# Kernel tuning notes

Hardware: AMD Instinct MI355X
Metric: run time of the kernel (lower is better)

## Reference

```python
import jax, jax.numpy as jnp
import numpy as np

MU = 5
ETA = 1.0
ITERATIONS = 3


def _sobel(x):
    # torch F.conv2d is cross-correlation; replicate exactly
    k = jnp.array([[-1., 0., 1.], [-2., 0., 2.], [-1., 0., 1.]], dtype=x.dtype)
    kernel = jnp.stack([k, k.T])[:, None]  # [2,1,3,3] OIHW
    return jax.lax.conv_general_dilated(
        x, kernel, window_strides=(1, 1), padding=[(1, 1), (1, 1)],
        dimension_numbers=('NCHW', 'OIHW', 'NCHW'))


def _cnorm(v):
    # 2-norm over channel dim, keepdim
    return jnp.sqrt(jnp.sum(v * v, axis=1, keepdims=True))


def setup_inputs() -> dict:
    key = jax.random.key(0)
    inputs = jax.random.uniform(key, (8, 1, 1024, 1024), dtype=jnp.float32)
    return {"inputs": inputs}


def reference(inputs):
    B, _, H, W = inputs.shape
    pad = ((0, 0), (0, 0), (MU, MU), (MU, MU))

    sobel = _sobel(inputs)                       # [B,2,H,W]
    sobel_mag = _cnorm(sobel)                    # [B,1,H,W]
    sobel_mag = sobel_mag / jnp.max(sobel_mag)
    sobel_mag_p = jnp.pad(sobel_mag, pad)

    # tang = flip(sobel, ch) * [-1, 1] -> perpendicular (tangent) field
    tang = jnp.stack([-sobel[:, 1], sobel[:, 0]], axis=1)
    tmag = _cnorm(tang)
    tang = tang / jnp.where(tmag == 0, jnp.ones_like(tmag), tmag)

    for _it in range(ITERATIONS):
        for ori in ('V', 'H'):
            tang_p = jnp.pad(tang, pad)
            tang_X = tang
            acc = jnp.zeros_like(tang)
            for i in range(2 * MU + 1):
                if ori == 'V':
                    tang_Y = tang_p[:, :, i:i + H, MU:MU + W]
                    sob_Y = sobel_mag_p[:, :, i:i + H, MU:MU + W]
                else:
                    tang_Y = tang_p[:, :, MU:MU + H, i:i + W]
                    sob_Y = sobel_mag_p[:, :, MU:MU + H, i:i + W]
                w = (jnp.tanh(ETA * (sob_Y - sobel_mag)) + 1.0) \
                    * jnp.sum(tang_X * tang_Y, axis=1, keepdims=True) * 0.5
                acc = acc + tang_Y * w
            tang = acc
        tmag = _cnorm(tang)
        tang = tang / jnp.where(tmag == 0, jnp.ones_like(tmag), tmag)
    return tang
```

## Files before the change

### kernel.cpp

```cpp
#include <hip/hip_runtime.h>

#define MU 5
static constexpr int Hh = 1024, Ww = 1024, Bb = 8;
static constexpr int NPIX = Bb * Hh * Ww;
static constexpr int TPB = 256;
static constexpr int SPY = 4;
static constexpr int SOBEL_BLOCKS = NPIX / SPY / TPB;
static constexpr int PY = 8, PX = 8;
static constexpr int VBLK = NPIX / PY / TPB;
static constexpr int HBLK = NPIX / PX / TPB;

__device__ __forceinline__ float rcp_fast(float x) { return __builtin_amdgcn_rcpf(x); }
__device__ __forceinline__ float rsq_fast(float x) { return __builtin_amdgcn_rsqf(x); }

template <int NB>
__device__ __forceinline__ int xcd_swizzle(int bid) {
    return (bid & 7) * (NB / 8) + (bid >> 3);
}

__global__ __launch_bounds__(TPB) void sobel_kernel(
        const float* __restrict__ in, float2* __restrict__ tang,
        float* __restrict__ mag, float* __restrict__ partials) {
    int id = blockIdx.x * TPB + threadIdx.x;
    int x = id & (Ww - 1);
    int yg = (id >> 10) & (Hh / SPY - 1);
    int b = id >> 18;
    int y0 = yg * SPY;
    const float* p = in + ((size_t)b << 20);

    float a[SPY + 2][3];
    bool cl = (x > 0), cr = (x < Ww - 1);
    if (yg >= 1 && yg <= Hh / SPY - 2) {
        #pragma unroll
        for (int r = 0; r < SPY + 2; ++r) {
            const float* row = p + (y0 - 1 + r) * Ww + x;
            a[r][0] = cl ? row[-1] : 0.0f;
            a[r][1] = row[0];
            a[r][2] = cr ? row[1] : 0.0f;
        }
    } else {
        #pragma unroll
        for (int r = 0; r < SPY + 2; ++r) {
            int yy = y0 - 1 + r;
            bool okr = (yy >= 0) && (yy < Hh);
            const float* row = p + (okr ? yy : 0) * Ww + x;
            a[r][0] = (okr && cl) ? row[-1] : 0.0f;
            a[r][1] = okr ? row[0] : 0.0f;
            a[r][2] = (okr && cr) ? row[1] : 0.0f;
        }
    }

    float s[SPY + 2];
    #pragma unroll
    for (int r = 0; r < SPY + 2; ++r) s[r] = a[r][2] - a[r][0];

    float vmax = 0.0f;
    #pragma unroll
    for (int k = 0; k < SPY; ++k) {
        float gx = s[k] + 2.0f * s[k + 1] + s[k + 2];
        float u1 = a[k + 2][0] - a[k][0];
        float u2 = a[k + 2][1] - a[k][1];
        float u3 = a[k + 2][2] - a[k][2];
        float gy = u1 + 2.0f * u2 + u3;
        float g2 = gx * gx + gy * gy;
        float irs = rsq_fast(g2);
        float m   = (g2 > 0.0f) ? g2 * irs : 0.0f;
        float inv = (g2 > 0.0f) ? irs : 1.0f;
        int j = (b << 20) + (y0 + k) * Ww + x;
        mag[j] = m;
        tang[j] = make_float2(-gy * inv, gx * inv);
        vmax = fmaxf(vmax, m);
    }

    #pragma unroll
    for (int off = 32; off; off >>= 1) vmax = fmaxf(vmax, __shfl_xor(vmax, off));
    __shared__ float smax[4];
    int lane = threadIdx.x & 63, wid = threadIdx.x >> 6;
    if (lane == 0) smax[wid] = vmax;
    __syncthreads();
    if (threadIdx.x == 0)
        partials[blockIdx.x] = fmaxf(fmaxf(smax[0], smax[1]), fmaxf(smax[2], smax[3]));
}

__global__ void max_reduce_kernel(const float* __restrict__ partials,
                                  float* __restrict__ scale_out) {
    float v = 0.0f;
    for (int i = threadIdx.x; i < SOBEL_BLOCKS; i += 1024)
        v = fmaxf(v, partials[i]);
    #pragma unroll
    for (int off = 32; off; off >>= 1) v = fmaxf(v, __shfl_xor(v, off));
    __shared__ float smax[16];
    int lane = threadIdx.x & 63, wid = threadIdx.x >> 6;
    if (lane == 0) smax[wid] = v;
    __syncthreads();
    if (threadIdx.x == 0) {
        float m = smax[0];
        #pragma unroll
        for (int i = 1; i < 16; ++i) m = fmaxf(m, smax[i]);
        *scale_out = 1.0f / m;
    }
}

__global__ void prep_kernel(float4* __restrict__ mag4,
                            const float* __restrict__ scalep) {
    int id = blockIdx.x * blockDim.x + threadIdx.x;
    float k = 2.0f * (*scalep);
    float4 m = mag4[id];
    m.x = __expf(k * m.x);
    m.y = __expf(k * m.y);
    m.z = __expf(k * m.z);
    m.w = __expf(k * m.w);
    mag4[id] = m;
}

__global__ __launch_bounds__(TPB) void etf_v(const float2* __restrict__ src,
                                             float2* __restrict__ dst,
                                             const float* __restrict__ E) {
    int bid = xcd_swizzle<VBLK>((int)blockIdx.x);
    int gid = bid * TPB + threadIdx.x;
    int x = gid & (Ww - 1);
    int yg = (gid >> 10) & (Hh / PY - 1);
    int b = gid >> 17;
    int y0 = yg * PY;
    int base = b << 20;

    float2 t[PY + 10];
    float  e[PY + 10];
    if (yg >= 1 && yg <= Hh / PY - 2) {
        #pragma unroll
        for (int r = 0; r < PY + 10; ++r) {
            int j = base + (y0 - MU + r) * Ww + x;
            t[r] = src[j];
            e[r] = E[j];
        }
    } else {
        #pragma unroll
        for (int r = 0; r < PY + 10; ++r) {
            int row = y0 - MU + r;
            bool ok = (row >= 0) && (row < Hh);
            int j = base + (ok ? row : 0) * Ww + x;
            t[r] = ok ? src[j] : make_float2(0.0f, 0.0f);
            e[r] = ok ? E[j] : 1.0f;
        }
    }

    #pragma unroll
    for (int k = 0; k < PY; ++k) {
        float2 tX = t[k + MU];
        float  eX = e[k + MU];
        float ax = 0.0f, ay = 0.0f;
        #pragma unroll
        for (int i = 0; i <= 2 * MU; ++i) {
            float2 tY = t[k + i];
            float  eY = e[k + i];
            float d = tX.x * tY.x + tX.y * tY.y;
            float w = eY * rcp_fast(eX + eY) * d;
            ax += tY.x * w;
            ay += tY.y * w;
        }
        dst[base + (y0 + k) * Ww + x] = make_float2(ax, ay);
    }
}

template <bool FINAL>
__global__ __launch_bounds__(TPB) void etf_h(const float2* __restrict__ src,
                                             float2* __restrict__ dstI,
                                             float* __restrict__ dstP,
                                             const float* __restrict__ E) {
    int bid = xcd_swizzle<HBLK>((int)blockIdx.x);
    int gid = bid * TPB + threadIdx.x;
    int xq = gid & (Ww / PX - 1);
    int x0 = xq * PX;
    int y = (gid >> 7) & (Hh - 1);
    int b = gid >> 17;
    int rowbase = (b << 20) + y * Ww;

    float2 t[PX + 10];
    float  e[PX + 10];
    if (xq >= 1 && xq <= Ww / PX - 2) {
        #pragma unroll
        for (int r = 0; r < PX + 10; ++r) {
            int j = rowbase + x0 - MU + r;
            t[r] = src[j];
            e[r] = E[j];
        }
    } else {
        #pragma unroll
        for (int r = 0; r < PX + 10; ++r) {
            int col = x0 - MU + r;
            bool ok = (col >= 0) && (col < Ww);
            int j = rowbase + (ok ? col : 0);
            t[r] = ok ? src[j] : make_float2(0.0f, 0.0f);
            e[r] = ok ? E[j] : 1.0f;
        }
    }

    float ox[PX], oy[PX];
    #pragma unroll
    for (int k = 0; k < PX; ++k) {
        float2 tX = t[k + MU];
        float  eX = e[k + MU];
        float ax = 0.0f, ay = 0.0f;
        #pragma unroll
        for (int i = 0; i <= 2 * MU; ++i) {
            float2 tY = t[k + i];
            float  eY = e[k + i];
            float d = tX.x * tY.x + tX.y * tY.y;
            float w = eY * rcp_fast(eX + eY) * d;
            ax += tY.x * w;
            ay += tY.y * w;
        }
        float n2 = ax * ax + ay * ay;
        float inv = (n2 > 0.0f) ? rsq_fast(n2) : 1.0f;
        ox[k] = ax * inv;
        oy[k] = ay * inv;
    }

    if (FINAL) {
        float4* px = (float4*)&dstP[((size_t)(b * 2 + 0) << 20) + y * Ww + x0];
        px[0] = make_float4(ox[0], ox[1], ox[2], ox[3]);
        px[1] = make_float4(ox[4], ox[5], ox[6], ox[7]);
        float4* py = (float4*)&dstP[((size_t)(b * 2 + 1) << 20) + y * Ww + x0];
        py[0] = make_float4(oy[0], oy[1], oy[2], oy[3]);
        py[1] = make_float4(oy[4], oy[5], oy[6], oy[7]);
    } else {
        float4* dp = (float4*)&dstI[rowbase + x0];
        dp[0] = make_float4(ox[0], oy[0], ox[1], oy[1]);
        dp[1] = make_float4(ox[2], oy[2], ox[3], oy[3]);
        dp[2] = make_float4(ox[4], oy[4], ox[5], oy[5]);
        dp[3] = make_float4(ox[6], oy[6], ox[7], oy[7]);
    }
}

extern "C" void kernel_launch(void* const* d_in, const int* in_sizes, int n_in,
                              void* d_out, int out_size, void* d_ws, size_t ws_size,
                              hipStream_t stream) {
    const float* in = (const float*)d_in[0];
    float* out = (float*)d_out;
    char* ws = (char*)d_ws;

    float* magE = (float*)ws;
    float2* tA = (float2*)(ws + (size_t)NPIX * sizeof(float));
    float* partials = (float*)(ws + (size_t)NPIX * sizeof(float)
                                  + (size_t)NPIX * sizeof(float2));
    float* scalep = partials + SOBEL_BLOCKS;
    float2* tOut = (float2*)out;

    sobel_kernel<<<SOBEL_BLOCKS, TPB, 0, stream>>>(in, tOut, magE, partials);
    max_reduce_kernel<<<1, 1024, 0, stream>>>(partials, scalep);
    prep_kernel<<<NPIX / 4 / TPB, TPB, 0, stream>>>((float4*)magE, scalep);

    etf_v<<<VBLK, TPB, 0, stream>>>(tOut, tA, magE);
    etf_h<false><<<HBLK, TPB, 0, stream>>>(tA, tOut, nullptr, magE);
    etf_v<<<VBLK, TPB, 0, stream>>>(tOut, tA, magE);
    etf_h<false><<<HBLK, TPB, 0, stream>>>(tA, tOut, nullptr, magE);
    etf_v<<<VBLK, TPB, 0, stream>>>(tOut, tA, magE);
    etf_h<true ><<<HBLK, TPB, 0, stream>>>(tA, nullptr, out, magE);
}
```

Before: 235.5 us.

## Fuse vertical and horizontal ETF passes into one tiled shared-memory kernel

Replaces the separate vertical and horizontal ETF kernels with one kernel per iteration that works on a 64x32 tile. It computes the vertical pass into LDS over a halo-widened column range, then runs the horizontal pass and normalisation from LDS. This removes the intermediate global write and read of the tangent field between passes and halves the launch count. In exchange it recomputes halo columns, adds LDS traffic and barriers, and writes through LDS to get coalesced stores. Buffer roles are swapped so the final result still lands in the output.

After: 259.8 us. 10.3% more time.

```diff
diff --git a/kernel.cpp b/kernel.cpp
--- a/kernel.cpp
+++ b/kernel.cpp
@@ -6,17 +6,15 @@
 static constexpr int TPB = 256;
 static constexpr int SPY = 4;
 static constexpr int SOBEL_BLOCKS = NPIX / SPY / TPB;
-static constexpr int PY = 8, PX = 8;
-static constexpr int VBLK = NPIX / PY / TPB;
-static constexpr int HBLK = NPIX / PX / TPB;
+
+static constexpr int TX = 64, TY = 32;
+static constexpr int VW = TX + 2 * MU;
+static constexpr int ER = TY + 2 * MU;
+static constexpr int EPITCH = 76;
+static constexpr int FBLK = (Ww / TX) * (Hh / TY) * Bb;
 
 __device__ __forceinline__ float rcp_fast(float x) { return __builtin_amdgcn_rcpf(x); }
 __device__ __forceinline__ float rsq_fast(float x) { return __builtin_amdgcn_rsqf(x); }
-
-template <int NB>
-__device__ __forceinline__ int xcd_swizzle(int bid) {
-    return (bid & 7) * (NB / 8) + (bid >> 3);
-}
 
 __global__ __launch_bounds__(TPB) void sobel_kernel(
         const float* __restrict__ in, float2* __restrict__ tang,
@@ -113,122 +111,121 @@
     mag4[id] = m;
 }
 
-__global__ __launch_bounds__(TPB) void etf_v(const float2* __restrict__ src,
-                                             float2* __restrict__ dst,
-                                             const float* __restrict__ E) {
-    int bid = xcd_swizzle<VBLK>((int)blockIdx.x);
-    int gid = bid * TPB + threadIdx.x;
-    int x = gid & (Ww - 1);
-    int yg = (gid >> 10) & (Hh / PY - 1);
-    int b = gid >> 17;
-    int y0 = yg * PY;
-    int base = b << 20;
-
-    float2 t[PY + 10];
-    float  e[PY + 10];
-    if (yg >= 1 && yg <= Hh / PY - 2) {
-        #pragma unroll
-        for (int r = 0; r < PY + 10; ++r) {
-            int j = base + (y0 - MU + r) * Ww + x;
-            t[r] = src[j];
-            e[r] = E[j];
-        }
-    } else {
-        #pragma unroll
-        for (int r = 0; r < PY + 10; ++r) {
-            int row = y0 - MU + r;
-            bool ok = (row >= 0) && (row < Hh);
-            int j = base + (ok ? row : 0) * Ww + x;
-            t[r] = ok ? src[j] : make_float2(0.0f, 0.0f);
-            e[r] = ok ? E[j] : 1.0f;
-        }
-    }
-
-    #pragma unroll
-    for (int k = 0; k < PY; ++k) {
-        float2 tX = t[k + MU];
-        float  eX = e[k + MU];
+template <bool FINAL>
+__global__ __launch_bounds__(TPB) void etf_fused(const float2* __restrict__ src,
+                                                 float2* __restrict__ dstI,
+                                                 float* __restrict__ dstP,
+                                                 const float* __restrict__ E) {
+    __shared__ float2 vT[TY][VW];
+    __shared__ float  eT[ER][EPITCH];
+
+    int bid = (int)blockIdx.x;
+    int swz = (bid & 7) * (FBLK / 8) + (bid >> 3);
+    int img = swz >> 9;
+    int cid = swz & 511;
+    int tx = cid >> 5, ty = cid & 31;
+    int x0 = tx * TX, y0 = ty * TY;
+    int base = img << 20;
+    int t = threadIdx.x;
+
+    for (int i = t; i < ER * VW; i += TPB) {
+        int r = i / VW, c = i % VW;
+        int gy = y0 - MU + r, gx = x0 - MU + c;
+        bool ok = (gy >= 0) && (gy < Hh) && (gx >= 0) && (gx < Ww);
+        eT[r][c] = ok ? E[base + gy * Ww + gx] : 1.0f;
+    }
+    __syncthreads();
+
+    for (int task = t; task < VW * (TY / 8); task += TPB) {
+        int c = task % VW;
+        int g = task / VW;
+        int gx = x0 - MU + c;
+        int yb = y0 + g * 8;
+        if (gx < 0 || gx >= Ww) {
+            #pragma unroll
+            for (int k = 0; k < 8; ++k) vT[g * 8 + k][c] = make_float2(0.0f, 0.0f);
+            continue;
+        }
+        float2 tt[18]; float ee[18];
+        if (yb - MU >= 0 && yb + 13 <= Hh) {
+            #pragma unroll
+            for (int rr = 0; rr < 18; ++rr) {
+                tt[rr] = src[base + (yb - MU + rr) * Ww + gx];
+                ee[rr] = eT[8 * g + rr][c];
+            }
+        } else {
+            #pragma unroll
+            for (int rr = 0; rr < 18; ++rr) {
+                int row = yb - MU + rr;
+                bool ok = (row >= 0) && (row < Hh);
+                tt[rr] = ok ? src[base + row * Ww + gx] : make_float2(0.0f, 0.0f);
+                ee[rr] = ok ? eT[8 * g + rr][c] : 1.0f;
+            }
+        }
+        #pragma unroll
+        for (int k = 0; k < 8; ++k) {
+            float2 tX = tt[k + MU];
+            float  eX = ee[k + MU];
+            float ax = 0.0f, ay = 0.0f;
+            #pragma unroll
+            for (int i = 0; i <= 2 * MU; ++i) {
+                float2 tY = tt[k + i];
+                float  eY = ee[k + i];
+                float d = tX.x * tY.x + tX.y * tY.y;
+                float w = eY * rcp_fast(eX + eY) * d;
+                ax += tY.x * w;
+                ay += tY.y * w;
+            }
+            vT[g * 8 + k][c] = make_float2(ax, ay);
+        }
+    }
+    __syncthreads();
+
+    int r = t >> 3;
+    int cb = (t & 7) * 8;
+    float2 wv[18]; float we[18];
+    #pragma unroll
+    for (int q = 0; q < 18; ++q) {
+        wv[q] = vT[r][cb + q];
+        we[q] = eT[r + MU][cb + q];
+    }
+    float ox[8], oy[8];
+    #pragma unroll
+    for (int j = 0; j < 8; ++j) {
+        float2 tX = wv[j + MU];
+        float  eX = we[j + MU];
         float ax = 0.0f, ay = 0.0f;
         #pragma unroll
         for (int i = 0; i <= 2 * MU; ++i) {
-            float2 tY = t[k + i];
-            float  eY = e[k + i];
+            float2 tY = wv[j + i];
+            float  eY = we[j + i];
             float d = tX.x * tY.x + tX.y * tY.y;
             float w = eY * rcp_fast(eX + eY) * d;
             ax += tY.x * w;
             ay += tY.y * w;
         }
-        dst[base + (y0 + k) * Ww + x] = make_float2(ax, ay);
-    }
-}
-
-template <bool FINAL>
-__global__ __launch_bounds__(TPB) void etf_h(const float2* __restrict__ src,
-                                             float2* __restrict__ dstI,
-                                             float* __restrict__ dstP,
-                                             const float* __restrict__ E) {
-    int bid = xcd_swizzle<HBLK>((int)blockIdx.x);
-    int gid = bid * TPB + threadIdx.x;
-    int xq = gid & (Ww / PX - 1);
-    int x0 = xq * PX;
-    int y = (gid >> 7) & (Hh - 1);
-    int b = gid >> 17;
-    int rowbase = (b << 20) + y * Ww;
-
-    float2 t[PX + 10];
-    float  e[PX + 10];
-    if (xq >= 1 && xq <= Ww / PX - 2) {
-        #pragma unroll
-        for (int r = 0; r < PX + 10; ++r) {
-            int j = rowbase + x0 - MU + r;
-            t[r] = src[j];
-            e[r] = E[j];
-        }
-    } else {
-        #pragma unroll
-        for (int r = 0; r < PX + 10; ++r) {
-            int col = x0 - MU + r;
-            bool ok = (col >= 0) && (col < Ww);
-            int j = rowbase + (ok ? col : 0);
-            t[r] = ok ? src[j] : make_float2(0.0f, 0.0f);
-            e[r] = ok ? E[j] : 1.0f;
-        }
-    }
-
-    float ox[PX], oy[PX];
-    #pragma unroll
-    for (int k = 0; k < PX; ++k) {
-        float2 tX = t[k + MU];
-        float  eX = e[k + MU];
-        float ax = 0.0f, ay = 0.0f;
-        #pragma unroll
-        for (int i = 0; i <= 2 * MU; ++i) {
-            float2 tY = t[k + i];
-            float  eY = e[k + i];
-            float d = tX.x * tY.x + tX.y * tY.y;
-            float w = eY * rcp_fast(eX + eY) * d;
-            ax += tY.x * w;
-            ay += tY.y * w;
-        }
         float n2 = ax * ax + ay * ay;
         float inv = (n2 > 0.0f) ? rsq_fast(n2) : 1.0f;
-        ox[k] = ax * inv;
-        oy[k] = ay * inv;
+        ox[j] = ax * inv;
+        oy[j] = ay * inv;
     }
 
     if (FINAL) {
-        float4* px = (float4*)&dstP[((size_t)(b * 2 + 0) << 20) + y * Ww + x0];
-        px[0] = make_float4(ox[0], ox[1], ox[2], ox[3]);
-        px[1] = make_float4(ox[4], ox[5], ox[6], ox[7]);
-        float4* py = (float4*)&dstP[((size_t)(b * 2 + 1) << 20) + y * Ww + x0];
-        py[0] = make_float4(oy[0], oy[1], oy[2], oy[3]);
-        py[1] = make_float4(oy[4], oy[5], oy[6], oy[7]);
+        size_t p0 = ((size_t)(img * 2 + 0) << 20) + (size_t)(y0 + r) * Ww + x0 + cb;
+        size_t p1 = ((size_t)(img * 2 + 1) << 20) + (size_t)(y0 + r) * Ww + x0 + cb;
+        *(float4*)&dstP[p0]     = make_float4(ox[0], ox[1], ox[2], ox[3]);
+        *(float4*)&dstP[p0 + 4] = make_float4(ox[4], ox[5], ox[6], ox[7]);
+        *(float4*)&dstP[p1]     = make_float4(oy[0], oy[1], oy[2], oy[3]);
+        *(float4*)&dstP[p1 + 4] = make_float4(oy[4], oy[5], oy[6], oy[7]);
     } else {
-        float4* dp = (float4*)&dstI[rowbase + x0];
-        dp[0] = make_float4(ox[0], oy[0], ox[1], oy[1]);
-        dp[1] = make_float4(ox[2], oy[2], ox[3], oy[3]);
-        dp[2] = make_float4(ox[4], oy[4], ox[5], oy[5]);
-        dp[3] = make_float4(ox[6], oy[6], ox[7], oy[7]);
+        __syncthreads();
+        #pragma unroll
+        for (int j = 0; j < 8; ++j) vT[r][cb + j] = make_float2(ox[j], oy[j]);
+        __syncthreads();
+        for (int i = t; i < TY * TX; i += TPB) {
+            int rr = i >> 6, cc = i & 63;
+            dstI[base + (y0 + rr) * Ww + x0 + cc] = vT[rr][cc];
+        }
     }
 }
 
@@ -246,14 +243,11 @@
     float* scalep = partials + SOBEL_BLOCKS;
     float2* tOut = (float2*)out;
 
-    sobel_kernel<<<SOBEL_BLOCKS, TPB, 0, stream>>>(in, tOut, magE, partials);
+    sobel_kernel<<<SOBEL_BLOCKS, TPB, 0, stream>>>(in, tA, magE, partials);
     max_reduce_kernel<<<1, 1024, 0, stream>>>(partials, scalep);
     prep_kernel<<<NPIX / 4 / TPB, TPB, 0, stream>>>((float4*)magE, scalep);
 
-    etf_v<<<VBLK, TPB, 0, stream>>>(tOut, tA, magE);
-    etf_h<false><<<HBLK, TPB, 0, stream>>>(tA, tOut, nullptr, magE);
-    etf_v<<<VBLK, TPB, 0, stream>>>(tOut, tA, magE);
-    etf_h<false><<<HBLK, TPB, 0, stream>>>(tA, tOut, nullptr, magE);
-    etf_v<<<VBLK, TPB, 0, stream>>>(tOut, tA, magE);
-    etf_h<true ><<<HBLK, TPB, 0, stream>>>(tA, nullptr, out, magE);
-}
+    etf_fused<false><<<FBLK, TPB, 0, stream>>>(tA, tOut, nullptr, magE);
+    etf_fused<false><<<FBLK, TPB, 0, stream>>>(tOut, tA, nullptr, magE);
+    etf_fused<true ><<<FBLK, TPB, 0, stream>>>(tA, nullptr, out, magE);
+}
```
